# Performance work log

Measured on AMD Instinct MI355X. Metric: run time of the kernel, lower is better.

## Reference

```python
import jax, jax.numpy as jnp
import numpy as np

NUM_HEADS = 8
NUM_GROUPS = 32
EPS = 1e-5


def group_norm(x, gamma, beta):
    # x: [B, C, H, W]; normalize over (C//G, H, W) within each of G groups
    B, C, H, W = x.shape
    xg = x.reshape(B, NUM_GROUPS, C // NUM_GROUPS, H, W)
    mean = xg.mean(axis=(2, 3, 4), keepdims=True)
    var = xg.var(axis=(2, 3, 4), keepdims=True)
    xn = ((xg - mean) * jax.lax.rsqrt(var + EPS)).reshape(B, C, H, W)
    return xn * gamma[None, :, None, None] + beta[None, :, None, None]


def setup_inputs() -> dict:
    key = jax.random.key(0)
    ks = jax.random.split(key, 7)
    B, C, H, W = 16, 512, 32, 32
    x = jax.random.normal(ks[0], (B, C, H, W), dtype=jnp.float32)
    gamma = jnp.ones((C,), dtype=jnp.float32)
    beta = jnp.zeros((C,), dtype=jnp.float32)
    # 1x1 convs == per-pixel linear layers
    w_qkv = jax.random.normal(ks[1], (3 * C, C), dtype=jnp.float32) * (1.0 / np.sqrt(C))
    b_qkv = jax.random.normal(ks[2], (3 * C,), dtype=jnp.float32) * 0.02
    w_proj = jax.random.normal(ks[3], (C, C), dtype=jnp.float32) * (1.0 / np.sqrt(C))
    b_proj = jax.random.normal(ks[4], (C,), dtype=jnp.float32) * 0.02
    return {"x": x, "gamma": gamma, "beta": beta, "w_qkv": w_qkv,
            "b_qkv": b_qkv, "w_proj": w_proj, "b_proj": b_proj}


def reference(x, gamma, beta, w_qkv, b_qkv, w_proj, b_proj):
    B, C, H, W = x.shape
    nh = NUM_HEADS
    d = C // nh
    N = H * W
    h = group_norm(x, gamma, beta)
    # 1x1 conv: [B,C,H,W] x [3C,C] -> [B,3C,H,W]
    qkv = jnp.einsum('bchw,oc->bohw', h, w_qkv) + b_qkv[None, :, None, None]
    qkv = qkv.reshape(B, 3, nh, d, N)  # matches torch reshape(B,3,heads,d,HW)
    q, k, v = qkv[:, 0], qkv[:, 1], qkv[:, 2]
    scale = d ** (-0.5)
    attn = jnp.einsum('bhdn,bhdm->bhnm', q, k) * scale  # [B,h,N,N]
    attn = jax.nn.softmax(attn, axis=-1)
    out = jnp.einsum('bhnm,bhdm->bhdn', attn, v)  # [B,h,d,N]
    out = out.reshape(B, C, H, W)
    proj = jnp.einsum('bchw,oc->bohw', out, w_proj) + b_proj[None, :, None, None]
    return x + proj
```

## Files before the change

### kernel.cpp

```cpp
#include <hip/hip_runtime.h>
#include <cstddef>

#define B_  16
#define C_  512
#define N_  1024

typedef __attribute__((ext_vector_type(8))) __bf16 bf16x8;
typedef __attribute__((ext_vector_type(4))) float f32x4;
typedef __attribute__((ext_vector_type(4))) short s16x4;

__device__ __forceinline__ unsigned short f2bf(float x) {
  unsigned u = __float_as_uint(x);
  return (unsigned short)((u + 0x7fffu + ((u >> 16) & 1u)) >> 16);
}
__device__ __forceinline__ float bf2f(unsigned short h) {
  return __uint_as_float(((unsigned)h) << 16);
}

#define GLDS16(g, l)                                                            \
  __builtin_amdgcn_global_load_lds(                                             \
      (const __attribute__((address_space(1))) void*)(g),                       \
      (__attribute__((address_space(3))) void*)(l), 16, 0, 0)

__global__ __launch_bounds__(256) void wconv_kernel(
    const float* __restrict__ wq, const float* __restrict__ wp,
    unsigned short* __restrict__ oq, unsigned short* __restrict__ op) {
  int i = blockIdx.x * 256 + threadIdx.x;
  const float4* src; unsigned short* dst; int off;
  if (i < 196608) { src = (const float4*)wq; dst = oq; off = i; }
  else            { src = (const float4*)wp; dst = op; off = i - 196608; }
  float4 v = src[off];
  union { unsigned short s[4]; ushort4 u; } o;
  o.s[0] = f2bf(v.x); o.s[1] = f2bf(v.y);
  o.s[2] = f2bf(v.z); o.s[3] = f2bf(v.w);
  *(ushort4*)(dst + (size_t)off * 4) = o.u;
}

__global__ __launch_bounds__(256) void gn_kernel(
    const float* __restrict__ x, const float* __restrict__ gamma,
    const float* __restrict__ beta, unsigned short* __restrict__ hT) {
  int bg = blockIdx.x;
  int b = bg >> 5, g = bg & 31;
  size_t base = ((size_t)b * C_ + (size_t)g * 16) * N_;
  const float4* x4 = (const float4*)(x + base);
  int tid = threadIdx.x;

  float sum = 0.f, sq = 0.f;
  float4 vv[16];
#pragma unroll
  for (int i = 0; i < 16; i++) {
    float4 v = x4[tid + i * 256];
    vv[i] = v;
    sum += v.x + v.y + v.z + v.w;
    sq  += v.x * v.x + v.y * v.y + v.z * v.z + v.w * v.w;
  }
#pragma unroll
  for (int off = 32; off > 0; off >>= 1) {
    sum += __shfl_down(sum, off, 64);
    sq  += __shfl_down(sq, off, 64);
  }
  __shared__ float sm[4], sv[4];
  int lane = tid & 63, w = tid >> 6;
  if (lane == 0) { sm[w] = sum; sv[w] = sq; }
  __syncthreads();
  if (tid == 0) {
    float s = sm[0] + sm[1] + sm[2] + sm[3];
    float q = sv[0] + sv[1] + sv[2] + sv[3];
    float mean = s * (1.f / 16384.f);
    float var  = q * (1.f / 16384.f) - mean * mean;
    sm[0] = mean;
    sv[0] = rsqrtf(var + 1e-5f);
  }
  __syncthreads();
  float mean = sm[0], rstd = sv[0];

  union { unsigned short s[16]; uint4 u[2]; } row[4];
#pragma unroll
  for (int i = 0; i < 16; i++) {
    int c = g * 16 + i;
    float ga = gamma[c] * rstd;
    float be = beta[c] - mean * ga;
    float4 v = vv[i];
    row[0].s[i] = f2bf(v.x * ga + be);
    row[1].s[i] = f2bf(v.y * ga + be);
    row[2].s[i] = f2bf(v.z * ga + be);
    row[3].s[i] = f2bf(v.w * ga + be);
  }
#pragma unroll
  for (int j = 0; j < 4; j++) {
    uint4* dst = (uint4*)(hT + ((size_t)b * N_ + 4 * tid + j) * C_ + g * 16);
    dst[0] = row[j].u[0];
    dst[1] = row[j].u[1];
  }
}

template <int OUT_BF16>
__global__ __launch_bounds__(256) void gemm_mfma(
    const unsigned short* __restrict__ Wb, const float* __restrict__ bias,
    const unsigned short* __restrict__ InT, const float* __restrict__ resid,
    void* __restrict__ Out, int M) {
  __shared__ __align__(16) unsigned short As[128 * 32];
  __shared__ __align__(16) unsigned short Bs[128 * 32];

  const int b = blockIdx.z;
  const int n0 = blockIdx.x * 128, m0 = blockIdx.y * 128;
  const int tid = threadIdx.x;
  const int lane = tid & 63, wave = tid >> 6;
  const int col = lane & 15, quad = lane >> 4;
  const int wm = (wave >> 1) << 6, wn = (wave & 1) << 6;

  const unsigned short* Ag = Wb + (size_t)m0 * C_;
  const unsigned short* Bg = InT + ((size_t)b * N_ + n0) * C_;

  const int r0 = tid >> 2, c0 = (tid & 3) << 3;

  f32x4 acc[4][4];
#pragma unroll
  for (int i = 0; i < 4; i++)
#pragma unroll
    for (int j = 0; j < 4; j++) acc[i][j] = f32x4{0.f, 0.f, 0.f, 0.f};

  for (int k0 = 0; k0 < C_; k0 += 32) {
    __syncthreads();
    GLDS16(Ag + (size_t)r0 * C_ + k0 + c0,        &As[tid * 8]);
    GLDS16(Ag + (size_t)(r0 + 64) * C_ + k0 + c0, &As[(tid + 256) * 8]);
    GLDS16(Bg + (size_t)r0 * C_ + k0 + c0,        &Bs[tid * 8]);
    GLDS16(Bg + (size_t)(r0 + 64) * C_ + k0 + c0, &Bs[(tid + 256) * 8]);
    __syncthreads();

    bf16x8 af[4], bfr[4];
#pragma unroll
    for (int mt = 0; mt < 4; mt++)
      af[mt] = *(const bf16x8*)&As[(wm + mt * 16 + col) * 32 + quad * 8];
#pragma unroll
    for (int nt = 0; nt < 4; nt++)
      bfr[nt] = *(const bf16x8*)&Bs[(wn + nt * 16 + col) * 32 + quad * 8];
#pragma unroll
    for (int mt = 0; mt < 4; mt++)
#pragma unroll
      for (int nt = 0; nt < 4; nt++)
        acc[mt][nt] = __builtin_amdgcn_mfma_f32_16x16x32_bf16(
            af[mt], bfr[nt], acc[mt][nt], 0, 0, 0);
  }

  const bool kT = OUT_BF16 && (m0 >= 512) && (m0 < 1024);

#pragma unroll
  for (int mt = 0; mt < 4; mt++) {
    int mbase = m0 + wm + mt * 16 + quad * 4;
#pragma unroll
    for (int nt = 0; nt < 4; nt++) {
      int n = n0 + wn + nt * 16 + col;
      if constexpr (OUT_BF16) {
        if (kT) {
          union { unsigned short s[4]; ushort4 v; } o;
#pragma unroll
          for (int r = 0; r < 4; r++)
            o.s[r] = f2bf(acc[mt][nt][r] + bias[mbase + r]);
          unsigned short* kt_out =
              (unsigned short*)Out + ((size_t)b * 1536 + 512) * N_;
          *(ushort4*)(kt_out + (size_t)n * 512 + (mbase - 512)) = o.v;
        } else {
#pragma unroll
          for (int r = 0; r < 4; r++) {
            float v = acc[mt][nt][r] + bias[mbase + r];
            ((unsigned short*)Out)[((size_t)b * M + mbase + r) * N_ + n] = f2bf(v);
          }
        }
      } else {
#pragma unroll
        for (int r = 0; r < 4; r++) {
          int m = mbase + r;
          float v = acc[mt][nt][r] + bias[m];
          size_t off = ((size_t)b * M + m) * N_ + n;
          ((float*)Out)[off] = v + resid[off];
        }
      }
    }
  }
}

__device__ __forceinline__ void attn_tile(const bf16x8 (&qf)[4][2],
                                          const bf16x8 (&kf)[4][2],
                                          const s16x4 (&vf)[4][4],
                                          f32x4 (&O)[4][4], float (&l_i)[4]) {
#pragma unroll
  for (int nt = 0; nt < 4; nt++) {
    f32x4 sf[4];
#pragma unroll
    for (int mt = 0; mt < 4; mt++) sf[mt] = f32x4{0.f, 0.f, 0.f, 0.f};
    __builtin_amdgcn_s_setprio(1);
#pragma unroll
    for (int ks = 0; ks < 2; ks++)
#pragma unroll
      for (int mt = 0; mt < 4; mt++)
        sf[mt] = __builtin_amdgcn_mfma_f32_16x16x32_bf16(
            kf[mt][ks], qf[nt][ks], sf[mt], 0, 0, 0);
    __builtin_amdgcn_s_setprio(0);

    s16x4 pb[4];
    float lsum = 0.f;
#pragma unroll
    for (int kc = 0; kc < 4; kc++) {
      float e0 = __expf(sf[kc][0]);
      float e1 = __expf(sf[kc][1]);
      float e2 = __expf(sf[kc][2]);
      float e3 = __expf(sf[kc][3]);
      lsum += (e0 + e1) + (e2 + e3);
      unsigned lo = __builtin_amdgcn_perm(__float_as_uint(e1), __float_as_uint(e0), 0x07060302u);
      unsigned hi = __builtin_amdgcn_perm(__float_as_uint(e3), __float_as_uint(e2), 0x07060302u);
      union { unsigned u[2]; s16x4 v; } t;
      t.u[0] = lo; t.u[1] = hi;
      pb[kc] = t.v;
    }
    l_i[nt] += lsum;

    __builtin_amdgcn_s_setprio(1);
#pragma unroll
    for (int kc = 0; kc < 4; kc++)
#pragma unroll
      for (int mt = 0; mt < 4; mt++)
        O[mt][nt] = __builtin_amdgcn_mfma_f32_16x16x16bf16_1k(
            vf[mt][kc], pb[kc], O[mt][nt], 0, 0, 0);
    __builtin_amdgcn_s_setprio(0);
  }
}

__global__ __launch_bounds__(256, 2) void attn_mfma(
    const unsigned short* __restrict__ qkv, unsigned short* __restrict__ aoT) {
  __shared__ __align__(16) unsigned short KtL[2][64 * 64];
  __shared__ __align__(16) unsigned short VsL[2][64 * 64];

  const int tid = threadIdx.x;
  const int wave = tid >> 6, lane = tid & 63;
  const int quad = lane >> 4, col = lane & 15;
  const int b = blockIdx.z, hh = blockIdx.y;
  const int qblk = blockIdx.x * 256 + wave * 64;

  const unsigned short* qp  = qkv + ((size_t)b * 1536 + hh * 64) * N_;
  const unsigned short* ktp = qkv + ((size_t)b * 1536 + 512) * N_ + hh * 64;
  const unsigned short* vp  = qkv + ((size_t)b * 1536 + 1024 + hh * 64) * N_;

  const int sr = tid >> 3;
  const int sw8 = (((tid & 7) ^ (sr & 7)) << 3);

  bf16x8 qf[4][2];
#pragma unroll
  for (int nt = 0; nt < 4; nt++) {
    int qg = qblk + nt * 16 + col;
#pragma unroll
    for (int ks = 0; ks < 2; ks++) {
      union { unsigned short s[8]; bf16x8 v; } t;
#pragma unroll
      for (int j = 0; j < 8; j++) {
        int d = ks * 32 + quad * 8 + j;
        t.s[j] = f2bf(0.125f * bf2f(qp[(size_t)d * N_ + qg]));
      }
      qf[nt][ks] = t.v;
    }
  }

  float l_i[4];
  f32x4 O[4][4];
#pragma unroll
  for (int nt = 0; nt < 4; nt++) {
    l_i[nt] = 0.f;
#pragma unroll
    for (int mt = 0; mt < 4; mt++) O[mt][nt] = f32x4{0.f, 0.f, 0.f, 0.f};
  }

  {
    const unsigned short* kq = ktp + (size_t)sr * 512 + sw8;
    GLDS16(kq,                    &KtL[0][tid * 8]);
    GLDS16(kq + (size_t)32 * 512, &KtL[0][(256 + tid) * 8]);
    const unsigned short* vq = vp + (size_t)sr * N_ + sw8;
    GLDS16(vq,                    &VsL[0][tid * 8]);
    GLDS16(vq + (size_t)32 * N_,  &VsL[0][(256 + tid) * 8]);
  }
  __syncthreads();

  for (int kt = 0; kt < 16; kt++) {
    const int cur = kt & 1;
    if (kt < 15) {
      const unsigned short* kq = ktp + (size_t)((kt + 1) * 64 + sr) * 512 + sw8;
      GLDS16(kq,                    &KtL[cur ^ 1][tid * 8]);
      GLDS16(kq + (size_t)32 * 512, &KtL[cur ^ 1][(256 + tid) * 8]);
      const unsigned short* vq = vp + (size_t)sr * N_ + (kt + 1) * 64 + sw8;
      GLDS16(vq,                    &VsL[cur ^ 1][tid * 8]);
      GLDS16(vq + (size_t)32 * N_,  &VsL[cur ^ 1][(256 + tid) * 8]);
    }

    bf16x8 kf[4][2];
#pragma unroll
    for (int mt = 0; mt < 4; mt++) {
      int key = 16 * mt + col;
#pragma unroll
      for (int ks = 0; ks < 2; ks++)
        kf[mt][ks] = *(const bf16x8*)
            &KtL[cur][key * 64 + (((ks * 4 + quad) ^ (col & 7)) << 3)];
    }
    s16x4 vf[4][4];
#pragma unroll
    for (int mt = 0; mt < 4; mt++) {
      int d = 16 * mt + col;
#pragma unroll
      for (int kc = 0; kc < 4; kc++)
        vf[mt][kc] = *(const s16x4*)
            &VsL[cur][d * 64 + (((kc * 4 + quad) ^ ((col & 7) << 1)) << 2)];
    }

    attn_tile(qf, kf, vf, O, l_i);

    if (kt < 15) __syncthreads();
  }

#pragma unroll
  for (int nt = 0; nt < 4; nt++) {
    float ls = l_i[nt];
    ls += __shfl_xor(ls, 16, 64);
    ls += __shfl_xor(ls, 32, 64);
    float inv = 1.f / ls;
    int qg = qblk + nt * 16 + col;
    unsigned short* dst = aoT + ((size_t)b * N_ + qg) * C_ + hh * 64;
#pragma unroll
    for (int mt = 0; mt < 4; mt++) {
      union { unsigned short s[4]; ushort4 v; } o;
#pragma unroll
      for (int r = 0; r < 4; r++) o.s[r] = f2bf(O[mt][nt][r] * inv);
      *(ushort4*)(dst + mt * 16 + quad * 4) = o.v;
    }
  }
}

extern "C" void kernel_launch(void* const* d_in, const int* in_sizes, int n_in,
                              void* d_out, int out_size, void* d_ws, size_t ws_size,
                              hipStream_t stream) {
  (void)in_sizes; (void)n_in; (void)out_size; (void)ws_size;
  const float* x      = (const float*)d_in[0];
  const float* gamma  = (const float*)d_in[1];
  const float* beta   = (const float*)d_in[2];
  const float* w_qkv  = (const float*)d_in[3];
  const float* b_qkv  = (const float*)d_in[4];
  const float* w_proj = (const float*)d_in[5];
  const float* b_proj = (const float*)d_in[6];
  float* out = (float*)d_out;

  unsigned short* hT   = (unsigned short*)d_ws;
  unsigned short* qkvb = hT + (size_t)B_ * N_ * C_;
  unsigned short* aoT  = hT;
  unsigned short* wqb  = qkvb + (size_t)B_ * 1536 * N_;
  unsigned short* wpb  = wqb + (size_t)1536 * 512;

  wconv_kernel<<<dim3(1024), dim3(256), 0, stream>>>(w_qkv, w_proj, wqb, wpb);
  gn_kernel<<<dim3(B_ * 32), dim3(256), 0, stream>>>(x, gamma, beta, hT);
  gemm_mfma<1><<<dim3(8, 12, 16), dim3(256), 0, stream>>>(
      wqb, b_qkv, hT, (const float*)nullptr, (void*)qkvb, 1536);
  attn_mfma<<<dim3(4, 8, 16), dim3(256), 0, stream>>>(qkvb, aoT);
  gemm_mfma<0><<<dim3(8, 4, 16), dim3(256), 0, stream>>>(
      wpb, b_proj, aoT, x, (void*)out, 512);
}
```

Measured before the change: 223.7 us.

## Shrink attention query tile, pad LDS, and stage K-transpose epilogue through LDS

The attention kernel now gives each wave 32 queries instead of 64, launches 1024 blocks on a flat grid with heads varying fastest, and targets four blocks per CU. It also swaps the direct global-to-LDS loads with XOR swizzle for register-staged loads into padded LDS rows. The QKV GEMM now writes its transposed K output through a padded shared buffer, so global stores become coalesced 16-byte rows instead of scattered 8-byte writes. In exchange, each K/V tile is loaded and reused by fewer queries, there are more blocks, and there are extra syncs and LDS traffic.

```diff
diff --git a/kernel.cpp b/kernel.cpp
--- a/kernel.cpp
+++ b/kernel.cpp
@@ -99,8 +99,7 @@
     const unsigned short* __restrict__ Wb, const float* __restrict__ bias,
     const unsigned short* __restrict__ InT, const float* __restrict__ resid,
     void* __restrict__ Out, int M) {
-  __shared__ __align__(16) unsigned short As[128 * 32];
-  __shared__ __align__(16) unsigned short Bs[128 * 32];
+  __shared__ __align__(16) unsigned short SH[2][128 * 34];
 
   const int b = blockIdx.z;
   const int n0 = blockIdx.x * 128, m0 = blockIdx.y * 128;
@@ -122,19 +121,19 @@
 
   for (int k0 = 0; k0 < C_; k0 += 32) {
     __syncthreads();
-    GLDS16(Ag + (size_t)r0 * C_ + k0 + c0,        &As[tid * 8]);
-    GLDS16(Ag + (size_t)(r0 + 64) * C_ + k0 + c0, &As[(tid + 256) * 8]);
-    GLDS16(Bg + (size_t)r0 * C_ + k0 + c0,        &Bs[tid * 8]);
-    GLDS16(Bg + (size_t)(r0 + 64) * C_ + k0 + c0, &Bs[(tid + 256) * 8]);
+    GLDS16(Ag + (size_t)r0 * C_ + k0 + c0,        &SH[0][tid * 8]);
+    GLDS16(Ag + (size_t)(r0 + 64) * C_ + k0 + c0, &SH[0][(tid + 256) * 8]);
+    GLDS16(Bg + (size_t)r0 * C_ + k0 + c0,        &SH[1][tid * 8]);
+    GLDS16(Bg + (size_t)(r0 + 64) * C_ + k0 + c0, &SH[1][(tid + 256) * 8]);
     __syncthreads();
 
     bf16x8 af[4], bfr[4];
 #pragma unroll
     for (int mt = 0; mt < 4; mt++)
-      af[mt] = *(const bf16x8*)&As[(wm + mt * 16 + col) * 32 + quad * 8];
+      af[mt] = *(const bf16x8*)&SH[0][(wm + mt * 16 + col) * 32 + quad * 8];
 #pragma unroll
     for (int nt = 0; nt < 4; nt++)
-      bfr[nt] = *(const bf16x8*)&Bs[(wn + nt * 16 + col) * 32 + quad * 8];
+      bfr[nt] = *(const bf16x8*)&SH[1][(wn + nt * 16 + col) * 32 + quad * 8];
 #pragma unroll
     for (int mt = 0; mt < 4; mt++)
 #pragma unroll
@@ -145,6 +144,40 @@
 
   const bool kT = OUT_BF16 && (m0 >= 512) && (m0 < 1024);
 
+  if (kT) {
+    unsigned short* epi = &SH[0][0];
+    unsigned short* kt_out =
+        (unsigned short*)Out + ((size_t)b * 1536 + 512) * N_ + (m0 - 512);
+#pragma unroll
+    for (int hf = 0; hf < 2; hf++) {
+      __syncthreads();
+      if ((wave & 1) == hf) {
+#pragma unroll
+        for (int mt = 0; mt < 4; mt++) {
+          int mloc = wm + mt * 16 + quad * 4;
+          int mabs = m0 + mloc;
+#pragma unroll
+          for (int nt = 0; nt < 4; nt++) {
+            union { unsigned short s[4]; ushort4 v; } o;
+#pragma unroll
+            for (int r = 0; r < 4; r++)
+              o.s[r] = f2bf(acc[mt][nt][r] + bias[mabs + r]);
+            *(ushort4*)&epi[(nt * 16 + col) * 136 + mloc] = o.v;
+          }
+        }
+      }
+      __syncthreads();
+#pragma unroll
+      for (int pass = 0; pass < 4; pass++) {
+        int n_l = (tid >> 4) + pass * 16;
+        int ch = tid & 15;
+        uint4 v = *(const uint4*)&epi[n_l * 136 + ch * 8];
+        *(uint4*)(kt_out + (size_t)(n0 + hf * 64 + n_l) * 512 + ch * 8) = v;
+      }
+    }
+    return;
+  }
+
 #pragma unroll
   for (int mt = 0; mt < 4; mt++) {
     int mbase = m0 + wm + mt * 16 + quad * 4;
@@ -152,20 +185,10 @@
     for (int nt = 0; nt < 4; nt++) {
       int n = n0 + wn + nt * 16 + col;
       if constexpr (OUT_BF16) {
-        if (kT) {
-          union { unsigned short s[4]; ushort4 v; } o;
-#pragma unroll
-          for (int r = 0; r < 4; r++)
-            o.s[r] = f2bf(acc[mt][nt][r] + bias[mbase + r]);
-          unsigned short* kt_out =
-              (unsigned short*)Out + ((size_t)b * 1536 + 512) * N_;
-          *(ushort4*)(kt_out + (size_t)n * 512 + (mbase - 512)) = o.v;
-        } else {
-#pragma unroll
-          for (int r = 0; r < 4; r++) {
-            float v = acc[mt][nt][r] + bias[mbase + r];
-            ((unsigned short*)Out)[((size_t)b * M + mbase + r) * N_ + n] = f2bf(v);
-          }
+#pragma unroll
+        for (int r = 0; r < 4; r++) {
+          float v = acc[mt][nt][r] + bias[mbase + r];
+          ((unsigned short*)Out)[((size_t)b * M + mbase + r) * N_ + n] = f2bf(v);
         }
       } else {
 #pragma unroll
@@ -180,12 +203,12 @@
   }
 }
 
-__device__ __forceinline__ void attn_tile(const bf16x8 (&qf)[4][2],
+__device__ __forceinline__ void attn_tile(const bf16x8 (&qf)[2][2],
                                           const bf16x8 (&kf)[4][2],
                                           const s16x4 (&vf)[4][4],
-                                          f32x4 (&O)[4][4], float (&l_i)[4]) {
-#pragma unroll
-  for (int nt = 0; nt < 4; nt++) {
+                                          f32x4 (&O)[4][2], float (&l_i)[2]) {
+#pragma unroll
+  for (int nt = 0; nt < 2; nt++) {
     f32x4 sf[4];
 #pragma unroll
     for (int mt = 0; mt < 4; mt++) sf[mt] = f32x4{0.f, 0.f, 0.f, 0.f};
@@ -226,27 +249,27 @@
   }
 }
 
-__global__ __launch_bounds__(256, 2) void attn_mfma(
+__global__ __launch_bounds__(256, 4) void attn_mfma(
     const unsigned short* __restrict__ qkv, unsigned short* __restrict__ aoT) {
-  __shared__ __align__(16) unsigned short KtL[2][64 * 64];
-  __shared__ __align__(16) unsigned short VsL[2][64 * 64];
+  __shared__ __align__(16) unsigned short Kt[2][64 * 72];
+  __shared__ __align__(16) unsigned short Vs[2][64 * 68];
 
   const int tid = threadIdx.x;
   const int wave = tid >> 6, lane = tid & 63;
   const int quad = lane >> 4, col = lane & 15;
-  const int b = blockIdx.z, hh = blockIdx.y;
-  const int qblk = blockIdx.x * 256 + wave * 64;
+  const int bi = blockIdx.x;
+  const int hh = bi & 7, qb = (bi >> 3) & 7, b = bi >> 6;
+  const int qblk = qb * 128 + wave * 32;
 
   const unsigned short* qp  = qkv + ((size_t)b * 1536 + hh * 64) * N_;
   const unsigned short* ktp = qkv + ((size_t)b * 1536 + 512) * N_ + hh * 64;
   const unsigned short* vp  = qkv + ((size_t)b * 1536 + 1024 + hh * 64) * N_;
 
-  const int sr = tid >> 3;
-  const int sw8 = (((tid & 7) ^ (sr & 7)) << 3);
-
-  bf16x8 qf[4][2];
-#pragma unroll
-  for (int nt = 0; nt < 4; nt++) {
+  const int sr0 = tid >> 3, sc0 = tid & 7;
+
+  bf16x8 qf[2][2];
+#pragma unroll
+  for (int nt = 0; nt < 2; nt++) {
     int qg = qblk + nt * 16 + col;
 #pragma unroll
     for (int ks = 0; ks < 2; ks++) {
@@ -260,34 +283,44 @@
     }
   }
 
-  float l_i[4];
-  f32x4 O[4][4];
-#pragma unroll
-  for (int nt = 0; nt < 4; nt++) {
+  float l_i[2];
+  f32x4 O[4][2];
+#pragma unroll
+  for (int nt = 0; nt < 2; nt++) {
     l_i[nt] = 0.f;
 #pragma unroll
     for (int mt = 0; mt < 4; mt++) O[mt][nt] = f32x4{0.f, 0.f, 0.f, 0.f};
   }
 
+  uint4 kr0, kr1, vr0, vr1;
   {
-    const unsigned short* kq = ktp + (size_t)sr * 512 + sw8;
-    GLDS16(kq,                    &KtL[0][tid * 8]);
-    GLDS16(kq + (size_t)32 * 512, &KtL[0][(256 + tid) * 8]);
-    const unsigned short* vq = vp + (size_t)sr * N_ + sw8;
-    GLDS16(vq,                    &VsL[0][tid * 8]);
-    GLDS16(vq + (size_t)32 * N_,  &VsL[0][(256 + tid) * 8]);
+    const unsigned short* kg = ktp + (size_t)sr0 * 512 + sc0 * 8;
+    kr0 = *(const uint4*)kg;
+    kr1 = *(const uint4*)(kg + (size_t)32 * 512);
+    const unsigned short* vg = vp + (size_t)sr0 * N_ + sc0 * 8;
+    vr0 = *(const uint4*)vg;
+    vr1 = *(const uint4*)(vg + (size_t)32 * N_);
+    *(uint4*)&Kt[0][sr0 * 72 + sc0 * 8] = kr0;
+    *(uint4*)&Kt[0][(sr0 + 32) * 72 + sc0 * 8] = kr1;
+    union { uint4 q; ushort4 h[2]; } u;
+    u.q = vr0;
+    *(ushort4*)&Vs[0][sr0 * 68 + sc0 * 8]     = u.h[0];
+    *(ushort4*)&Vs[0][sr0 * 68 + sc0 * 8 + 4] = u.h[1];
+    u.q = vr1;
+    *(ushort4*)&Vs[0][(sr0 + 32) * 68 + sc0 * 8]     = u.h[0];
+    *(ushort4*)&Vs[0][(sr0 + 32) * 68 + sc0 * 8 + 4] = u.h[1];
   }
   __syncthreads();
 
   for (int kt = 0; kt < 16; kt++) {
     const int cur = kt & 1;
     if (kt < 15) {
-      const unsigned short* kq = ktp + (size_t)((kt + 1) * 64 + sr) * 512 + sw8;
-      GLDS16(kq,                    &KtL[cur ^ 1][tid * 8]);
-      GLDS16(kq + (size_t)32 * 512, &KtL[cur ^ 1][(256 + tid) * 8]);
-      const unsigned short* vq = vp + (size_t)sr * N_ + (kt + 1) * 64 + sw8;
-      GLDS16(vq,                    &VsL[cur ^ 1][tid * 8]);
-      GLDS16(vq + (size_t)32 * N_,  &VsL[cur ^ 1][(256 + tid) * 8]);
+      const unsigned short* kg = ktp + (size_t)((kt + 1) * 64 + sr0) * 512 + sc0 * 8;
+      kr0 = *(const uint4*)kg;
+      kr1 = *(const uint4*)(kg + (size_t)32 * 512);
+      const unsigned short* vg = vp + (size_t)sr0 * N_ + (kt + 1) * 64 + sc0 * 8;
+      vr0 = *(const uint4*)vg;
+      vr1 = *(const uint4*)(vg + (size_t)32 * N_);
     }
 
     bf16x8 kf[4][2];
@@ -296,8 +329,7 @@
       int key = 16 * mt + col;
 #pragma unroll
       for (int ks = 0; ks < 2; ks++)
-        kf[mt][ks] = *(const bf16x8*)
-            &KtL[cur][key * 64 + (((ks * 4 + quad) ^ (col & 7)) << 3)];
+        kf[mt][ks] = *(const bf16x8*)&Kt[cur][key * 72 + ks * 32 + quad * 8];
     }
     s16x4 vf[4][4];
 #pragma unroll
@@ -305,17 +337,28 @@
       int d = 16 * mt + col;
 #pragma unroll
       for (int kc = 0; kc < 4; kc++)
-        vf[mt][kc] = *(const s16x4*)
-            &VsL[cur][d * 64 + (((kc * 4 + quad) ^ ((col & 7) << 1)) << 2)];
+        vf[mt][kc] = *(const s16x4*)&Vs[cur][d * 68 + kc * 16 + quad * 4];
     }
 
     attn_tile(qf, kf, vf, O, l_i);
 
-    if (kt < 15) __syncthreads();
-  }
-
-#pragma unroll
-  for (int nt = 0; nt < 4; nt++) {
+    if (kt < 15) {
+      const int nb = cur ^ 1;
+      *(uint4*)&Kt[nb][sr0 * 72 + sc0 * 8] = kr0;
+      *(uint4*)&Kt[nb][(sr0 + 32) * 72 + sc0 * 8] = kr1;
+      union { uint4 q; ushort4 h[2]; } u;
+      u.q = vr0;
+      *(ushort4*)&Vs[nb][sr0 * 68 + sc0 * 8]     = u.h[0];
+      *(ushort4*)&Vs[nb][sr0 * 68 + sc0 * 8 + 4] = u.h[1];
+      u.q = vr1;
+      *(ushort4*)&Vs[nb][(sr0 + 32) * 68 + sc0 * 8]     = u.h[0];
+      *(ushort4*)&Vs[nb][(sr0 + 32) * 68 + sc0 * 8 + 4] = u.h[1];
+      __syncthreads();
+    }
+  }
+
+#pragma unroll
+  for (int nt = 0; nt < 2; nt++) {
     float ls = l_i[nt];
     ls += __shfl_xor(ls, 16, 64);
     ls += __shfl_xor(ls, 32, 64);
@@ -355,7 +398,7 @@
   gn_kernel<<<dim3(B_ * 32), dim3(256), 0, stream>>>(x, gamma, beta, hT);
   gemm_mfma<1><<<dim3(8, 12, 16), dim3(256), 0, stream>>>(
       wqb, b_qkv, hT, (const float*)nullptr, (void*)qkvb, 1536);
-  attn_mfma<<<dim3(4, 8, 16), dim3(256), 0, stream>>>(qkvb, aoT);
+  attn_mfma<<<dim3(1024), dim3(256), 0, stream>>>(qkvb, aoT);
   gemm_mfma<0><<<dim3(8, 4, 16), dim3(256), 0, stream>>>(
       wpb, b_proj, aoT, x, (void*)out, 512);
 }
```

Measured after the change: 301.8 us. 34.9% more time.
